# Kernel optimization log

Measured on AMD Instinct MI355X. Metric: run time of the kernel, lower is better.

The kernel has to match this reference:

```python
import jax, jax.numpy as jnp
import numpy as np

EPS_LN = 1e-6
EPS_BN = 1e-5
NUM_HEADS = 8


def _dwconv(img, w, b=None, stride=1):
    # img: (B,C,H,W), w: (C,1,k,k) depthwise
    out = jax.lax.conv_general_dilated(
        img, w, (stride, stride), 'SAME',
        feature_group_count=img.shape[1],
        dimension_numbers=('NCHW', 'OIHW', 'NCHW'))
    if b is not None:
        out = out + b[None, :, None, None]
    return out


def _layernorm(x, g, b):
    m = jnp.mean(x, axis=-1, keepdims=True)
    v = jnp.mean(jnp.square(x - m), axis=-1, keepdims=True)
    return (x - m) * jax.lax.rsqrt(v + EPS_LN) * g + b


def _hardswish(x):
    return x * jnp.clip(x + 3.0, 0.0, 6.0) * (1.0 / 6.0)


def _forward(img, domain_label, pe_dw_w, pe_pw_w, pe_bn_g, pe_bn_b, pe_bn_m, pe_bn_v,
             cpe_w, cpe_b, norm1_g, norm1_b, qkv_w, qkv_b,
             crpe_w3, crpe_b3, crpe_w5, crpe_b5, crpe_w7, crpe_b7,
             dom_w1, dom_b1, dom_w2, dom_b2, proj_w, proj_b,
             norm2_g, norm2_b, fc1_w, fc1_b, fc2_w, fc2_b, d):
    B = img.shape[0]
    # --- DWCPatchEmbed_M: depthwise 3x3 s2 + pointwise 1x1 + domain BN (eval) + hardswish ---
    x = _dwconv(img, pe_dw_w, None, stride=2)                      # (B,Cin,H,W)
    x = jax.lax.conv_general_dilated(x, pe_pw_w, (1, 1), 'SAME',
                                     dimension_numbers=('NCHW', 'OIHW', 'NCHW'))
    g, be, mu, var = pe_bn_g[d], pe_bn_b[d], pe_bn_m[d], pe_bn_v[d]
    scale_bn = g * jax.lax.rsqrt(var + EPS_BN)
    x = (x - mu[None, :, None, None]) * scale_bn[None, :, None, None] + be[None, :, None, None]
    x = _hardswish(x)
    _, C, H, W = x.shape
    N = H * W
    x = x.reshape(B, C, N).transpose(0, 2, 1)                      # (B,N,C) tokens

    # --- ConvPosEnc: depthwise 3x3 on image layout, residual ---
    img2 = x.transpose(0, 2, 1).reshape(B, C, H, W)
    x = x + _dwconv(img2, cpe_w, cpe_b).reshape(B, C, N).transpose(0, 2, 1)

    # --- FactorAtt_ConvRelPosEnc_Sup ---
    cur = _layernorm(x, norm1_g[d], norm1_b[d])
    h = NUM_HEADS
    Ch = C // h
    qkv = cur @ qkv_w + qkv_b                                      # (B,N,3C)
    qkv = qkv.reshape(B, N, 3, h, Ch).transpose(2, 0, 3, 1, 4)     # (3,B,h,N,Ch)
    q, k, v = qkv[0], qkv[1], qkv[2]
    k_sm = jax.nn.softmax(k, axis=2)                               # softmax over tokens
    kv = jnp.einsum('bhnk,bhnv->bhkv', k_sm, v)                    # (B,h,Ch,Ch)
    factor_att = jnp.einsum('bhnk,bhkv->bhnv', q, kv)              # (B,h,N,Ch)

    # conv relative position encoding: windows {3:2heads, 5:3heads, 7:3heads}
    v_img = v.transpose(0, 1, 3, 2).reshape(B, C, H, W)            # (B, h*Ch, H, W)
    s1, s2 = 2 * Ch, 5 * Ch
    cv = jnp.concatenate([
        _dwconv(v_img[:, :s1], crpe_w3, crpe_b3),
        _dwconv(v_img[:, s1:s2], crpe_w5, crpe_b5),
        _dwconv(v_img[:, s2:], crpe_w7, crpe_b7)], axis=1)
    cv = cv.reshape(B, h, Ch, N).transpose(0, 1, 3, 2)             # (B,h,N,Ch)
    crpe = q * cv

    factor_att = (Ch ** -0.5) * factor_att + crpe

    # domain gate: Linear->ReLU->Linear on one-hot, softmax over heads
    da = jax.nn.relu(domain_label @ dom_w1 + dom_b1) @ dom_w2 + dom_b2   # (B,C)
    da = da.reshape(B, h, Ch)[:, :, None, :]                        # (B,h,1,Ch)
    da = jax.nn.softmax(da, axis=1)
    out = da * factor_att                                           # (B,h,N,Ch)
    out = out.transpose(0, 2, 1, 3).reshape(B, N, C)
    out = out @ proj_w + proj_b
    x = x + out

    # --- MLP (ratio 8), domain LayerNorm, residual ---
    cur = _layernorm(x, norm2_g[d], norm2_b[d])
    cur = jax.nn.gelu(cur @ fc1_w + fc1_b, approximate=False) @ fc2_w + fc2_b
    x = x + cur
    return x


def setup_inputs() -> dict:
    key = jax.random.key(0)
    ks = jax.random.split(key, 16)
    B, Cin, Hin, Win = 8, 64, 128, 128
    C, h, D = 128, NUM_HEADS, 4
    Ch = C // h
    hid_dom = C // 2
    hid_mlp = 8 * C
    f = jnp.float32

    def n(k, shape, s=0.02):
        return (s * jax.random.normal(k, shape)).astype(f)

    img = jax.random.normal(ks[0], (B, Cin, Hin, Win), dtype=f)
    domain_label = jax.nn.one_hot(jnp.zeros((B,), jnp.int32), D, dtype=f)
    return dict(
        img=img, domain_label=domain_label,
        pe_dw_w=n(ks[1], (Cin, 1, 3, 3), 0.1),
        pe_pw_w=n(ks[2], (C, Cin, 1, 1), 0.1),
        pe_bn_g=jnp.ones((D, C), f), pe_bn_b=jnp.zeros((D, C), f),
        pe_bn_m=n(ks[3], (D, C), 0.1),
        pe_bn_v=jnp.ones((D, C), f),
        cpe_w=n(ks[4], (C, 1, 3, 3), 0.1), cpe_b=jnp.zeros((C,), f),
        norm1_g=jnp.ones((D, C), f), norm1_b=jnp.zeros((D, C), f),
        qkv_w=n(ks[5], (C, 3 * C)), qkv_b=jnp.zeros((3 * C,), f),
        crpe_w3=n(ks[6], (2 * Ch, 1, 3, 3), 0.1), crpe_b3=jnp.zeros((2 * Ch,), f),
        crpe_w5=n(ks[7], (3 * Ch, 1, 5, 5), 0.1), crpe_b5=jnp.zeros((3 * Ch,), f),
        crpe_w7=n(ks[8], (3 * Ch, 1, 7, 7), 0.1), crpe_b7=jnp.zeros((3 * Ch,), f),
        dom_w1=n(ks[9], (D, hid_dom)), dom_b1=jnp.zeros((hid_dom,), f),
        dom_w2=n(ks[10], (hid_dom, C)), dom_b2=jnp.zeros((C,), f),
        proj_w=n(ks[11], (C, C)), proj_b=jnp.zeros((C,), f),
        norm2_g=jnp.ones((D, C), f), norm2_b=jnp.zeros((D, C), f),
        fc1_w=n(ks[12], (C, hid_mlp)), fc1_b=jnp.zeros((hid_mlp,), f),
        fc2_w=n(ks[13], (hid_mlp, C)), fc2_b=jnp.zeros((C,), f),
        d=0,
    )


def reference(img, domain_label, pe_dw_w, pe_pw_w, pe_bn_g, pe_bn_b, pe_bn_m, pe_bn_v,
              cpe_w, cpe_b, norm1_g, norm1_b, qkv_w, qkv_b,
              crpe_w3, crpe_b3, crpe_w5, crpe_b5, crpe_w7, crpe_b7,
              dom_w1, dom_b1, dom_w2, dom_b2, proj_w, proj_b,
              norm2_g, norm2_b, fc1_w, fc1_b, fc2_w, fc2_b, d):
    return _forward(img, domain_label, pe_dw_w, pe_pw_w, pe_bn_g, pe_bn_b, pe_bn_m, pe_bn_v,
                    cpe_w, cpe_b, norm1_g, norm1_b, qkv_w, qkv_b,
                    crpe_w3, crpe_b3, crpe_w5, crpe_b5, crpe_w7, crpe_b7,
                    dom_w1, dom_b1, dom_w2, dom_b2, proj_w, proj_b,
                    norm2_g, norm2_b, fc1_w, fc1_b, fc2_w, fc2_b, d)
```

## Files before the change

### kernel.cpp

```cpp
#include <hip/hip_runtime.h>
#include <math.h>

#define EPS_LN 1e-6f
#define EPS_BN 1e-5f

typedef __attribute__((ext_vector_type(8))) short bf16x8;
typedef __attribute__((ext_vector_type(4))) float f32x4;

__device__ __forceinline__ float wave_reduce_sum(float v) {
    #pragma unroll
    for (int m = 32; m >= 1; m >>= 1) v += __shfl_xor(v, m, 64);
    return v;
}
__device__ __forceinline__ float wave_reduce_max(float v) {
    #pragma unroll
    for (int m = 32; m >= 1; m >>= 1) v = fmaxf(v, __shfl_xor(v, m, 64));
    return v;
}
__device__ __forceinline__ short f2bf(float f) {
    union { float f; unsigned u; } v; v.f = f;
    unsigned r = v.u + 0x7fff + ((v.u >> 16) & 1);
    return (short)(r >> 16);
}
__device__ __forceinline__ unsigned pack2bf(float a, float b) {
    return (unsigned)(unsigned short)f2bf(a) | ((unsigned)(unsigned short)f2bf(b) << 16);
}

__global__ __launch_bounds__(256) void pe_kernel(
    const float* __restrict__ img, const float* __restrict__ dww,
    const float* __restrict__ pww, const float* __restrict__ bn_g,
    const float* __restrict__ bn_b, const float* __restrict__ bn_m,
    const float* __restrict__ bn_v, const int* __restrict__ dptr,
    float* __restrict__ t1) {
    __shared__ float dw[64 * 68];
    __shared__ float wsm[64 * 132];
    int bx = blockIdx.x;
    int b = bx >> 6, y = bx & 63;
    int tid = threadIdx.x;
    int d = *dptr;

    for (int idx = tid; idx < 8192; idx += 256) {
        int co = idx >> 6, ci = idx & 63;
        wsm[ci * 132 + co] = pww[idx];
    }

    for (int it = 0; it < 4; ++it) {
        int task = tid + it * 256;
        int ci = task >> 4, xx0 = (task & 15) * 4;
        const float* ip = img + (size_t)(b * 64 + ci) * 16384;
        const float* wd = dww + ci * 9;
        float a0 = 0.f, a1 = 0.f, a2 = 0.f, a3 = 0.f;
        #pragma unroll
        for (int r = 0; r < 3; ++r) {
            int iy = 2 * y + r;
            if (iy >= 128) continue;
            const float* rp = ip + iy * 128 + 2 * xx0;
            float u[9];
            *(f32x4*)&u[0] = *(const f32x4*)rp;
            *(f32x4*)&u[4] = *(const f32x4*)(rp + 4);
            u[8] = (xx0 < 60) ? rp[8] : 0.f;
            #pragma unroll
            for (int s = 0; s < 3; ++s) {
                float w = wd[r * 3 + s];
                a0 += u[s] * w;
                a1 += u[2 + s] * w;
                a2 += u[4 + s] * w;
                a3 += u[6 + s] * w;
            }
        }
        f32x4 st = {a0, a1, a2, a3};
        *(f32x4*)&dw[ci * 68 + xx0] = st;
    }
    __syncthreads();

    int xg = tid & 15, cog = tid >> 4;
    int xx0 = xg * 4, co0 = cog * 8;
    f32x4 acc[8];
    f32x4 zr = {0.f, 0.f, 0.f, 0.f};
    #pragma unroll
    for (int i = 0; i < 8; ++i) acc[i] = zr;
    for (int ci = 0; ci < 64; ++ci) {
        f32x4 dv = *(const f32x4*)&dw[ci * 68 + xx0];
        f32x4 w0 = *(const f32x4*)&wsm[ci * 132 + co0];
        f32x4 w1 = *(const f32x4*)&wsm[ci * 132 + co0 + 4];
        acc[0] += dv * w0.x; acc[1] += dv * w0.y;
        acc[2] += dv * w0.z; acc[3] += dv * w0.w;
        acc[4] += dv * w1.x; acc[5] += dv * w1.y;
        acc[6] += dv * w1.z; acc[7] += dv * w1.w;
    }
    #pragma unroll
    for (int i = 0; i < 8; ++i) {
        int co = co0 + i;
        float sc = bn_g[d * 128 + co] * rsqrtf(bn_v[d * 128 + co] + EPS_BN);
        float mu = bn_m[d * 128 + co], be = bn_b[d * 128 + co];
        f32x4 v = (acc[i] - mu) * sc + be;
        f32x4 r;
        r.x = v.x * fminf(fmaxf(v.x + 3.f, 0.f), 6.f) * (1.f / 6.f);
        r.y = v.y * fminf(fmaxf(v.y + 3.f, 0.f), 6.f) * (1.f / 6.f);
        r.z = v.z * fminf(fmaxf(v.z + 3.f, 0.f), 6.f) * (1.f / 6.f);
        r.w = v.w * fminf(fmaxf(v.w + 3.f, 0.f), 6.f) * (1.f / 6.f);
        *(f32x4*)&t1[(size_t)(b * 128 + co) * 4096 + y * 64 + xx0] = r;
    }
}

__global__ __launch_bounds__(256) void cpe_kernel(
    const float* __restrict__ t1, const float* __restrict__ cw,
    const float* __restrict__ cb, float* __restrict__ xout) {
    int bx = blockIdx.x;
    int cq = bx & 3, y = (bx >> 2) & 63, b = bx >> 8;
    int c0 = cq * 32;
    __shared__ float s[3 * 32 * 65];
    int tid = threadIdx.x;
    for (int idx = tid; idx < 3 * 32 * 64; idx += 256) {
        int xx = idx & 63;
        int cl = (idx >> 6) & 31;
        int dy = idx >> 11;
        int yy = y + dy - 1;
        float v = 0.f;
        if (yy >= 0 && yy < 64)
            v = t1[(size_t)(b * 128 + c0 + cl) * 4096 + yy * 64 + xx];
        s[(dy * 32 + cl) * 65 + xx] = v;
    }
    __syncthreads();
    for (int idx = tid; idx < 32 * 64; idx += 256) {
        int cl = idx & 31;
        int xx = idx >> 5;
        int c = c0 + cl;
        float center = s[(32 + cl) * 65 + xx];
        float acc = cb[c];
        #pragma unroll
        for (int dy = 0; dy < 3; ++dy) {
            #pragma unroll
            for (int dx = 0; dx < 3; ++dx) {
                int sx = xx + dx - 1;
                if (sx < 0 || sx >= 64) continue;
                acc += s[(dy * 32 + cl) * 65 + sx] * cw[c * 9 + dy * 3 + dx];
            }
        }
        xout[(size_t)(b * 4096 + y * 64 + xx) * 128 + c] = center + acc;
    }
}

__global__ __launch_bounds__(256) void pack_qkv_kernel(
    const float* __restrict__ w, const float* __restrict__ g,
    const int* __restrict__ dptr, short* __restrict__ wp) {
    int idx = blockIdx.x * 256 + threadIdx.x;
    int d = *dptr;
    int l = idx & 63, kk = (idx >> 6) & 3, n = idx >> 8;
    int k0 = kk * 32 + (l >> 4) * 8;
    int c = n * 16 + (l & 15);
    bf16x8 v;
    #pragma unroll
    for (int j = 0; j < 8; ++j)
        v[j] = f2bf(g[d * 128 + k0 + j] * w[(size_t)(k0 + j) * 384 + c]);
    *(bf16x8*)&wp[(size_t)idx * 8] = v;
}
__global__ __launch_bounds__(256) void pack_pw_kernel(
    const float* __restrict__ w, short* __restrict__ wp) {
    int idx = blockIdx.x * 256 + threadIdx.x;
    int l = idx & 63, kk = (idx >> 6) & 3, n = idx >> 8;
    int k0 = kk * 32 + (l >> 4) * 8;
    int c = n * 16 + (l & 15);
    bf16x8 v;
    #pragma unroll
    for (int j = 0; j < 8; ++j) v[j] = f2bf(w[(size_t)(k0 + j) * 128 + c]);
    *(bf16x8*)&wp[(size_t)idx * 8] = v;
}
__global__ __launch_bounds__(256) void pack_w1_kernel(
    const float* __restrict__ w1, const float* __restrict__ g,
    const int* __restrict__ dptr, short* __restrict__ w1p) {
    int idx = blockIdx.x * 256 + threadIdx.x;
    int d = *dptr;
    int l = idx & 63, kk = (idx >> 6) & 3, n = idx >> 8;
    int k0 = kk * 32 + (l >> 4) * 8;
    int c = n * 16 + (l & 15);
    bf16x8 v;
    #pragma unroll
    for (int j = 0; j < 8; ++j)
        v[j] = f2bf(g[d * 128 + k0 + j] * w1[(size_t)(k0 + j) * 1024 + c]);
    *(bf16x8*)&w1p[(size_t)idx * 8] = v;
}
__global__ __launch_bounds__(256) void pack_w2_kernel(
    const float* __restrict__ w2, short* __restrict__ w2p) {
    int idx = blockIdx.x * 256 + threadIdx.x;
    int l = idx & 63, kk = (idx >> 6) & 31, n = idx >> 11;
    int k0 = kk * 32 + (l >> 4) * 8;
    int c = n * 16 + (l & 15);
    bf16x8 v;
    #pragma unroll
    for (int j = 0; j < 8; ++j) v[j] = f2bf(w2[(size_t)(k0 + j) * 128 + c]);
    *(bf16x8*)&w2p[(size_t)idx * 8] = v;
}

__global__ __launch_bounds__(256) void fold_qkv_bias_kernel(
    const float* __restrict__ w, const float* __restrict__ bqkv,
    const float* __restrict__ beta, const int* __restrict__ dptr,
    float* __restrict__ bp) {
    int j = blockIdx.x * 256 + threadIdx.x;
    if (j >= 384) return;
    int d = *dptr;
    float s = bqkv[j];
    for (int k = 0; k < 128; ++k) s += beta[d * 128 + k] * w[(size_t)k * 384 + j];
    bp[j] = s;
}
__global__ __launch_bounds__(256) void fold_fc1_bias_kernel(
    const float* __restrict__ w, const float* __restrict__ b1,
    const float* __restrict__ beta, const int* __restrict__ dptr,
    float* __restrict__ bp) {
    int j = blockIdx.x * 256 + threadIdx.x;
    if (j >= 1024) return;
    int d = *dptr;
    float s = b1[j];
    for (int k = 0; k < 128; ++k) s += beta[d * 128 + k] * w[(size_t)k * 1024 + j];
    bp[j] = s;
}

__global__ __launch_bounds__(256, 2) void qkv_mfma_kernel(
    const float* __restrict__ x, const short* __restrict__ wp,
    const float* __restrict__ biasp, float* __restrict__ q_img,
    float* __restrict__ k_img, float* __restrict__ v_img) {
    int tb = blockIdx.x * 32;
    int tid = threadIdx.x;
    int lane = tid & 63, wv = tid >> 6;
    int lhi = lane >> 4, llo = lane & 15;
    int b = tb >> 12, n0 = tb & 4095;

    bf16x8 afr[2][4];
    #pragma unroll
    for (int tt = 0; tt < 2; ++tt) {
        f32x4 v0[4], v1[4];
        float sum = 0.f;
        #pragma unroll
        for (int kk = 0; kk < 4; ++kk) {
            const float* p = x + (size_t)(tb + tt * 16 + llo) * 128 + kk * 32 + lhi * 8;
            v0[kk] = *(const f32x4*)p;
            v1[kk] = *(const f32x4*)(p + 4);
            sum += v0[kk].x + v0[kk].y + v0[kk].z + v0[kk].w
                 + v1[kk].x + v1[kk].y + v1[kk].z + v1[kk].w;
        }
        sum += __shfl_xor(sum, 16, 64);
        sum += __shfl_xor(sum, 32, 64);
        float mean = sum * (1.f / 128.f);
        float vs = 0.f;
        #pragma unroll
        for (int kk = 0; kk < 4; ++kk) {
            f32x4 a = v0[kk], c = v1[kk];
            float d0 = a.x - mean, d1 = a.y - mean, d2 = a.z - mean, d3 = a.w - mean;
            float d4 = c.x - mean, d5 = c.y - mean, d6 = c.z - mean, d7 = c.w - mean;
            vs += d0*d0 + d1*d1 + d2*d2 + d3*d3 + d4*d4 + d5*d5 + d6*d6 + d7*d7;
        }
        vs += __shfl_xor(vs, 16, 64);
        vs += __shfl_xor(vs, 32, 64);
        float rs = rsqrtf(vs * (1.f / 128.f) + EPS_LN);
        #pragma unroll
        for (int kk = 0; kk < 4; ++kk) {
            bf16x8 o;
            o[0] = f2bf((v0[kk].x - mean) * rs);
            o[1] = f2bf((v0[kk].y - mean) * rs);
            o[2] = f2bf((v0[kk].z - mean) * rs);
            o[3] = f2bf((v0[kk].w - mean) * rs);
            o[4] = f2bf((v1[kk].x - mean) * rs);
            o[5] = f2bf((v1[kk].y - mean) * rs);
            o[6] = f2bf((v1[kk].z - mean) * rs);
            o[7] = f2bf((v1[kk].w - mean) * rs);
            afr[tt][kk] = o;
        }
    }

    f32x4 acc[6][2];
    f32x4 zr = {0.f, 0.f, 0.f, 0.f};
    #pragma unroll
    for (int i = 0; i < 6; ++i) { acc[i][0] = zr; acc[i][1] = zr; }

    #pragma unroll
    for (int i = 0; i < 6; ++i) {
        int nb = wv * 6 + i;
        #pragma unroll
        for (int kk = 0; kk < 4; ++kk) {
            bf16x8 wf = *(const bf16x8*)&wp[((size_t)(nb * 4 + kk) * 64 + lane) * 8];
            acc[i][0] = __builtin_amdgcn_mfma_f32_16x16x32_bf16(wf, afr[0][kk], acc[i][0], 0, 0, 0);
            acc[i][1] = __builtin_amdgcn_mfma_f32_16x16x32_bf16(wf, afr[1][kk], acc[i][1], 0, 0, 0);
        }
    }

    #pragma unroll
    for (int i = 0; i < 6; ++i) {
        int j0 = (wv * 6 + i) * 16;
        f32x4 bv = *(const f32x4*)(biasp + j0 + lhi * 4);
        float* dst = (j0 < 128) ? q_img : ((j0 < 256) ? k_img : v_img);
        int c0 = (j0 & 127) + lhi * 4;
        #pragma unroll
        for (int tt = 0; tt < 2; ++tt) {
            f32x4 r = acc[i][tt] + bv;
            float* p = dst + (size_t)(b * 128 + c0) * 4096 + n0 + tt * 16 + llo;
            p[0]        = r.x;
            p[4096]     = r.y;
            p[2 * 4096] = r.z;
            p[3 * 4096] = r.w;
        }
    }
}

__global__ __launch_bounds__(256) void softmax_kernel(float* __restrict__ k_img) {
    __shared__ float red[4];
    float* p = k_img + (size_t)blockIdx.x * 4096;
    int tid = threadIdx.x;
    float v[16];
    float mx = -1e30f;
    #pragma unroll
    for (int i = 0; i < 16; ++i) {
        v[i] = p[tid + i * 256];
        mx = fmaxf(mx, v[i]);
    }
    mx = wave_reduce_max(mx);
    int wid = tid >> 6, lane = tid & 63;
    if (lane == 0) red[wid] = mx;
    __syncthreads();
    mx = fmaxf(fmaxf(red[0], red[1]), fmaxf(red[2], red[3]));
    __syncthreads();
    float sum = 0.f;
    #pragma unroll
    for (int i = 0; i < 16; ++i) {
        v[i] = expf(v[i] - mx);
        sum += v[i];
    }
    sum = wave_reduce_sum(sum);
    if (lane == 0) red[wid] = sum;
    __syncthreads();
    float inv = 1.f / (red[0] + red[1] + red[2] + red[3]);
    #pragma unroll
    for (int i = 0; i < 16; ++i)
        p[tid + i * 256] = v[i] * inv;
}

__global__ __launch_bounds__(256) void kv_part_kernel(
    const float* __restrict__ k_img, const float* __restrict__ v_img,
    float* __restrict__ kvp) {
    __shared__ float ks[16 * 132], vs[16 * 132];
    int bc = blockIdx.x;
    int bh = bc >> 3, chunk = bc & 7;
    int b = bh >> 3, h = bh & 7;
    int tid = threadIdx.x;
    int ck = tid >> 4, cv = tid & 15;
    float acc = 0.f;
    const float* kp = k_img + (size_t)(b * 128 + h * 16) * 4096;
    const float* vp = v_img + (size_t)(b * 128 + h * 16) * 4096;
    int nb0 = chunk * 512;
    for (int nb = nb0; nb < nb0 + 512; nb += 128) {
        for (int idx = tid; idx < 2048; idx += 256) {
            int r = idx >> 7, col = idx & 127;
            ks[r * 132 + col] = kp[(size_t)r * 4096 + nb + col];
            vs[r * 132 + col] = vp[(size_t)r * 4096 + nb + col];
        }
        __syncthreads();
        for (int kk = 0; kk < 128; ++kk)
            acc += ks[ck * 132 + kk] * vs[cv * 132 + kk];
        __syncthreads();
    }
    kvp[(size_t)(chunk * 64 + bh) * 256 + ck * 16 + cv] = acc;
}
__global__ __launch_bounds__(256) void kv_reduce_kernel(
    const float* __restrict__ kvp, float* __restrict__ kv) {
    int i = blockIdx.x * 256 + threadIdx.x;
    float s = 0.f;
    #pragma unroll
    for (int c = 0; c < 8; ++c) s += kvp[(size_t)c * 16384 + i];
    kv[i] = s;
}

__global__ __launch_bounds__(256) void fa_kernel(
    const float* __restrict__ q_img, const float* __restrict__ kv,
    float* __restrict__ fa_img) {
    __shared__ float kvs[256];
    int bid = blockIdx.x;
    int bh = bid >> 4, chunk = bid & 15;
    int b = bh >> 3, h = bh & 7;
    int tid = threadIdx.x;
    kvs[tid] = kv[bh * 256 + tid];
    __syncthreads();
    int n = chunk * 256 + tid;
    const float* qp = q_img + (size_t)(b * 128 + h * 16) * 4096 + n;
    float qv[16];
    #pragma unroll
    for (int ck = 0; ck < 16; ++ck) qv[ck] = qp[(size_t)ck * 4096];
    float* fp = fa_img + (size_t)(b * 128 + h * 16) * 4096 + n;
    #pragma unroll
    for (int cv = 0; cv < 16; ++cv) {
        float s = 0.f;
        #pragma unroll
        for (int ck = 0; ck < 16; ++ck) s += qv[ck] * kvs[ck * 16 + cv];
        fp[(size_t)cv * 4096] = s;
    }
}

__global__ __launch_bounds__(256) void gate_kernel(
    const float* __restrict__ dl, const float* __restrict__ w1,
    const float* __restrict__ b1, const float* __restrict__ w2,
    const float* __restrict__ b2, float* __restrict__ da) {
    __shared__ float hid[512];
    __shared__ float raw[1024];
    int tid = threadIdx.x;
    for (int idx = tid; idx < 512; idx += 256) {
        int b = idx >> 6, jj = idx & 63;
        float a = b1[jj];
        #pragma unroll
        for (int dd = 0; dd < 4; ++dd)
            a += dl[b * 4 + dd] * w1[dd * 64 + jj];
        hid[idx] = fmaxf(a, 0.f);
    }
    __syncthreads();
    for (int idx = tid; idx < 1024; idx += 256) {
        int b = idx >> 7, c = idx & 127;
        float a = b2[c];
        for (int jj = 0; jj < 64; ++jj)
            a += hid[b * 64 + jj] * w2[jj * 128 + c];
        raw[idx] = a;
    }
    __syncthreads();
    if (tid < 128) {
        int b = tid >> 4, ch = tid & 15;
        float mx = -1e30f;
        #pragma unroll
        for (int hh = 0; hh < 8; ++hh)
            mx = fmaxf(mx, raw[b * 128 + hh * 16 + ch]);
        float e[8];
        float s = 0.f;
        #pragma unroll
        for (int hh = 0; hh < 8; ++hh) {
            e[hh] = expf(raw[b * 128 + hh * 16 + ch] - mx);
            s += e[hh];
        }
        float inv = 1.f / s;
        #pragma unroll
        for (int hh = 0; hh < 8; ++hh)
            da[b * 128 + hh * 16 + ch] = e[hh] * inv;
    }
}

template<int KC>
__device__ __forceinline__ void conv4(const float* __restrict__ s,
                                      const float* __restrict__ wsm,
                                      int y, int xx0, float* a4) {
    const int OFF = KC / 2;
    #pragma unroll
    for (int dy = 0; dy < KC; ++dy) {
        int sy = y + dy - OFF;
        if (sy < 0 || sy >= 64) continue;
        const float* r = s + sy * 72;
        float u[12];
        *(f32x4*)&u[0] = *(const f32x4*)&r[xx0];
        *(f32x4*)&u[4] = *(const f32x4*)&r[xx0 + 4];
        *(f32x4*)&u[8] = *(const f32x4*)&r[xx0 + 8];
        #pragma unroll
        for (int dx = 0; dx < KC; ++dx) {
            float w = wsm[dy * KC + dx];
            const int base = dx - OFF + 4;
            a4[0] += u[base + 0] * w;
            a4[1] += u[base + 1] * w;
            a4[2] += u[base + 2] * w;
            a4[3] += u[base + 3] * w;
        }
    }
}

__global__ __launch_bounds__(256) void att_kernel(
    const float* __restrict__ q_img, const float* __restrict__ v_img,
    const float* __restrict__ fa_img, const float* __restrict__ da,
    const float* __restrict__ w3, const float* __restrict__ b3,
    const float* __restrict__ w5, const float* __restrict__ b5,
    const float* __restrict__ w7, const float* __restrict__ b7,
    float* __restrict__ att) {
    __shared__ float s[64 * 72];
    __shared__ float wsm[49];
    int o = ((blockIdx.x & 7) << 7) | (blockIdx.x >> 3);
    int b = o >> 7, c = o & 127;
    int tid = threadIdx.x;
    const float* vp = v_img + (size_t)(b * 128 + c) * 4096;
    for (int idx = tid; idx < 4096; idx += 256) {
        int row = idx >> 6, xx = idx & 63;
        s[row * 72 + xx + 4] = vp[idx];
    }
    for (int idx = tid; idx < 512; idx += 256) {
        int row = idx >> 3, j = idx & 7;
        s[row * 72 + (j < 4 ? j : 64 + j)] = 0.f;
    }
    int kc; const float* wp; float bias;
    if (c < 32)      { kc = 3; wp = w3 + c * 9;         bias = b3[c]; }
    else if (c < 80) { kc = 5; wp = w5 + (c - 32) * 25; bias = b5[c - 32]; }
    else             { kc = 7; wp = w7 + (c - 80) * 49; bias = b7[c - 80]; }
    if (tid < kc * kc) wsm[tid] = wp[tid];
    float dac = da[b * 128 + c];
    size_t rowbase = (size_t)(b * 128 + c) * 4096;
    __syncthreads();
    for (int it = 0; it < 4; ++it) {
        int task = tid + it * 256;
        int y = task >> 4, xx0 = (task & 15) * 4;
        float a4[4] = {bias, bias, bias, bias};
        if (kc == 3)      conv4<3>(s, wsm, y, xx0, a4);
        else if (kc == 5) conv4<5>(s, wsm, y, xx0, a4);
        else              conv4<7>(s, wsm, y, xx0, a4);
        size_t base = rowbase + y * 64 + xx0;
        f32x4 fav = *(const f32x4*)&fa_img[base];
        f32x4 qv  = *(const f32x4*)&q_img[base];
        f32x4 cv4 = {a4[0], a4[1], a4[2], a4[3]};
        f32x4 r = (fav * 0.25f + qv * cv4) * dac;
        *(f32x4*)&att[base] = r;
    }
}

__global__ __launch_bounds__(256, 2) void proj_mfma_kernel(
    const float* __restrict__ att, const short* __restrict__ wp,
    const float* __restrict__ bias, const float* __restrict__ xres,
    float* __restrict__ out) {
    __shared__ float As[128 * 33];
    int tb = blockIdx.x * 32;
    int tid = threadIdx.x;
    int lane = tid & 63, wv = tid >> 6;
    int lhi = lane >> 4, llo = lane & 15;
    int b = tb >> 12, n0 = tb & 4095;

    for (int idx = tid; idx < 4096; idx += 256) {
        int c = idx >> 5, t = idx & 31;
        As[c * 33 + t] = att[(size_t)(b * 128 + c) * 4096 + n0 + t];
    }
    __syncthreads();

    bf16x8 afr[2][4];
    #pragma unroll
    for (int tt = 0; tt < 2; ++tt) {
        #pragma unroll
        for (int kk = 0; kk < 4; ++kk) {
            int c0 = kk * 32 + lhi * 8;
            int t = tt * 16 + llo;
            bf16x8 v;
            #pragma unroll
            for (int j = 0; j < 8; ++j) v[j] = f2bf(As[(c0 + j) * 33 + t]);
            afr[tt][kk] = v;
        }
    }

    f32x4 acc[2][2];
    f32x4 zr = {0.f, 0.f, 0.f, 0.f};
    #pragma unroll
    for (int i = 0; i < 2; ++i) { acc[i][0] = zr; acc[i][1] = zr; }

    #pragma unroll
    for (int i = 0; i < 2; ++i) {
        int nb = wv * 2 + i;
        #pragma unroll
        for (int kk = 0; kk < 4; ++kk) {
            bf16x8 wf = *(const bf16x8*)&wp[((size_t)(nb * 4 + kk) * 64 + lane) * 8];
            acc[i][0] = __builtin_amdgcn_mfma_f32_16x16x32_bf16(wf, afr[0][kk], acc[i][0], 0, 0, 0);
            acc[i][1] = __builtin_amdgcn_mfma_f32_16x16x32_bf16(wf, afr[1][kk], acc[i][1], 0, 0, 0);
        }
    }

    #pragma unroll
    for (int i = 0; i < 2; ++i) {
        int j0 = (wv * 2 + i) * 16;
        f32x4 bv = *(const f32x4*)(bias + j0 + lhi * 4);
        #pragma unroll
        for (int tt = 0; tt < 2; ++tt) {
            size_t o = (size_t)(tb + tt * 16 + llo) * 128 + j0 + lhi * 4;
            f32x4 xr = *(const f32x4*)(xres + o);
            *(f32x4*)(out + o) = xr + acc[i][tt] + bv;
        }
    }
}

__global__ __launch_bounds__(256, 2) void mlp_mfma_kernel(
    const short* __restrict__ w1p, const float* __restrict__ b1p,
    const short* __restrict__ w2p, const float* __restrict__ b2,
    float* io) {
    __shared__ short hs[32768];
    int tb = blockIdx.x * 32;
    int tid = threadIdx.x;
    int lane = tid & 63, wv = tid >> 6;
    int lhi = lane >> 4, llo = lane & 15;

    bf16x8 afr[2][4];
    #pragma unroll
    for (int tt = 0; tt < 2; ++tt) {
        f32x4 v0[4], v1[4];
        float sum = 0.f;
        #pragma unroll
        for (int kk = 0; kk < 4; ++kk) {
            const float* p = io + (size_t)(tb + tt * 16 + llo) * 128 + kk * 32 + lhi * 8;
            v0[kk] = *(const f32x4*)p;
            v1[kk] = *(const f32x4*)(p + 4);
            sum += v0[kk].x + v0[kk].y + v0[kk].z + v0[kk].w
                 + v1[kk].x + v1[kk].y + v1[kk].z + v1[kk].w;
        }
        sum += __shfl_xor(sum, 16, 64);
        sum += __shfl_xor(sum, 32, 64);
        float mean = sum * (1.f / 128.f);
        float vs = 0.f;
        #pragma unroll
        for (int kk = 0; kk < 4; ++kk) {
            f32x4 a = v0[kk], c = v1[kk];
            float d0 = a.x - mean, d1 = a.y - mean, d2 = a.z - mean, d3 = a.w - mean;
            float d4 = c.x - mean, d5 = c.y - mean, d6 = c.z - mean, d7 = c.w - mean;
            vs += d0*d0 + d1*d1 + d2*d2 + d3*d3 + d4*d4 + d5*d5 + d6*d6 + d7*d7;
        }
        vs += __shfl_xor(vs, 16, 64);
        vs += __shfl_xor(vs, 32, 64);
        float rs = rsqrtf(vs * (1.f / 128.f) + EPS_LN);
        #pragma unroll
        for (int kk = 0; kk < 4; ++kk) {
            bf16x8 o;
            o[0] = f2bf((v0[kk].x - mean) * rs);
            o[1] = f2bf((v0[kk].y - mean) * rs);
            o[2] = f2bf((v0[kk].z - mean) * rs);
            o[3] = f2bf((v0[kk].w - mean) * rs);
            o[4] = f2bf((v1[kk].x - mean) * rs);
            o[5] = f2bf((v1[kk].y - mean) * rs);
            o[6] = f2bf((v1[kk].z - mean) * rs);
            o[7] = f2bf((v1[kk].w - mean) * rs);
            afr[tt][kk] = o;
        }
    }

    f32x4 acc[2][16];
    f32x4 zr = {0.f, 0.f, 0.f, 0.f};
    #pragma unroll
    for (int tt = 0; tt < 2; ++tt)
        #pragma unroll
        for (int nl = 0; nl < 16; ++nl) acc[tt][nl] = zr;

    const short* wbase = w1p + (size_t)(wv * 16) * 4 * 64 * 8;
    #pragma unroll
    for (int nl = 0; nl < 16; ++nl) {
        #pragma unroll
        for (int kk = 0; kk < 4; ++kk) {
            bf16x8 bf = *(const bf16x8*)(wbase + ((size_t)(nl * 4 + kk) * 64 + lane) * 8);
            acc[0][nl] = __builtin_amdgcn_mfma_f32_16x16x32_bf16(bf, afr[0][kk], acc[0][nl], 0, 0, 0);
            acc[1][nl] = __builtin_amdgcn_mfma_f32_16x16x32_bf16(bf, afr[1][kk], acc[1][nl], 0, 0, 0);
        }
    }

    #pragma unroll
    for (int nl = 0; nl < 16; ++nl) {
        int hn = wv * 16 + nl;
        int hc0 = hn * 16 + lhi * 4;
        f32x4 bv = *(const f32x4*)(b1p + hc0);
        int kk2 = hn >> 1;
        int lp = llo + 16 * ((hn & 1) * 2 + (lhi >> 1));
        #pragma unroll
        for (int tt = 0; tt < 2; ++tt) {
            f32x4 a = acc[tt][nl] + bv;
            float g0 = 0.5f * a.x * (1.f + erff(a.x * 0.70710678118654752f));
            float g1 = 0.5f * a.y * (1.f + erff(a.y * 0.70710678118654752f));
            float g2 = 0.5f * a.z * (1.f + erff(a.z * 0.70710678118654752f));
            float g3 = 0.5f * a.w * (1.f + erff(a.w * 0.70710678118654752f));
            uint2 wv2;
            wv2.x = pack2bf(g0, g1);
            wv2.y = pack2bf(g2, g3);
            *(uint2*)((char*)hs + ((size_t)(tt * 32 + kk2) * 64 + lp) * 16 + (lhi & 1) * 8) = wv2;
        }
    }
    __syncthreads();

    f32x4 acc2[2][2];
    #pragma unroll
    for (int cn = 0; cn < 2; ++cn)
        #pragma unroll
        for (int tt = 0; tt < 2; ++tt) acc2[cn][tt] = zr;

    const short* w2base = w2p + (size_t)(wv * 2) * 32 * 64 * 8;
    #pragma unroll 4
    for (int kk2 = 0; kk2 < 32; ++kk2) {
        bf16x8 h0 = *(const bf16x8*)&hs[((size_t)(0 * 32 + kk2) * 64 + lane) * 8];
        bf16x8 h1 = *(const bf16x8*)&hs[((size_t)(1 * 32 + kk2) * 64 + lane) * 8];
        bf16x8 w0 = *(const bf16x8*)(w2base + ((size_t)(0 * 32 + kk2) * 64 + lane) * 8);
        bf16x8 w1f = *(const bf16x8*)(w2base + ((size_t)(1 * 32 + kk2) * 64 + lane) * 8);
        acc2[0][0] = __builtin_amdgcn_mfma_f32_16x16x32_bf16(w0, h0, acc2[0][0], 0, 0, 0);
        acc2[0][1] = __builtin_amdgcn_mfma_f32_16x16x32_bf16(w0, h1, acc2[0][1], 0, 0, 0);
        acc2[1][0] = __builtin_amdgcn_mfma_f32_16x16x32_bf16(w1f, h0, acc2[1][0], 0, 0, 0);
        acc2[1][1] = __builtin_amdgcn_mfma_f32_16x16x32_bf16(w1f, h1, acc2[1][1], 0, 0, 0);
    }

    #pragma unroll
    for (int cn = 0; cn < 2; ++cn) {
        int c0 = (wv * 2 + cn) * 16 + lhi * 4;
        f32x4 bv = *(const f32x4*)(b2 + c0);
        #pragma unroll
        for (int tt = 0; tt < 2; ++tt) {
            float* op = io + (size_t)(tb + tt * 16 + llo) * 128 + c0;
            f32x4 r = *(f32x4*)op;
            r = r + acc2[cn][tt] + bv;
            *(f32x4*)op = r;
        }
    }
}

extern "C" void kernel_launch(void* const* d_in, const int* in_sizes, int n_in,
                              void* d_out, int out_size, void* d_ws, size_t ws_size,
                              hipStream_t stream) {
    const float* img   = (const float*)d_in[0];
    const float* dl    = (const float*)d_in[1];
    const float* pe_dw = (const float*)d_in[2];
    const float* pe_pw = (const float*)d_in[3];
    const float* bn_g  = (const float*)d_in[4];
    const float* bn_b  = (const float*)d_in[5];
    const float* bn_m  = (const float*)d_in[6];
    const float* bn_v  = (const float*)d_in[7];
    const float* cpe_w = (const float*)d_in[8];
    const float* cpe_b = (const float*)d_in[9];
    const float* n1_g  = (const float*)d_in[10];
    const float* n1_b  = (const float*)d_in[11];
    const float* qkv_w = (const float*)d_in[12];
    const float* qkv_b = (const float*)d_in[13];
    const float* w3    = (const float*)d_in[14];
    const float* b3    = (const float*)d_in[15];
    const float* w5    = (const float*)d_in[16];
    const float* b5    = (const float*)d_in[17];
    const float* w7    = (const float*)d_in[18];
    const float* b7    = (const float*)d_in[19];
    const float* dw1   = (const float*)d_in[20];
    const float* db1   = (const float*)d_in[21];
    const float* dw2   = (const float*)d_in[22];
    const float* db2   = (const float*)d_in[23];
    const float* pw    = (const float*)d_in[24];
    const float* pb    = (const float*)d_in[25];
    const float* n2_g  = (const float*)d_in[26];
    const float* n2_b  = (const float*)d_in[27];
    const float* f1w   = (const float*)d_in[28];
    const float* f1b   = (const float*)d_in[29];
    const float* f2w   = (const float*)d_in[30];
    const float* f2b   = (const float*)d_in[31];
    const int*   dptr  = (const int*)d_in[32];
    float* out = (float*)d_out;

    char* ws = (char*)d_ws;
    const size_t SZ = (size_t)8 * 128 * 4096 * 4;
    float* t1    = (float*)(ws);
    float* x     = (float*)(ws + SZ);
    float* q_img = (float*)(ws + 2 * SZ);
    float* k_img = (float*)(ws + 3 * SZ);
    float* v_img = (float*)(ws + 4 * SZ);
    float* kv    = (float*)(ws + 5 * SZ);
    float* da    = (float*)(ws + 5 * SZ + 0x10000);
    short* qkvp  = (short*)(ws + 5 * SZ + 0x20000);
    short* pwp   = (short*)(ws + 5 * SZ + 0x40000);
    float* qbp   = (float*)(ws + 5 * SZ + 0x48000);
    float* f1bp  = (float*)(ws + 5 * SZ + 0x4A000);
    float* kvp   = (float*)(ws + 5 * SZ + 0x50000);
    float* fa_img = t1;
    short* w1p   = (short*)(ws + 2 * SZ);
    short* w2p   = (short*)(ws + 2 * SZ + 262144);

    pack_qkv_kernel<<<24, 256, 0, stream>>>(qkv_w, n1_g, dptr, qkvp);
    fold_qkv_bias_kernel<<<2, 256, 0, stream>>>(qkv_w, qkv_b, n1_b, dptr, qbp);
    pack_pw_kernel<<<8, 256, 0, stream>>>(pw, pwp);
    gate_kernel<<<1, 256, 0, stream>>>(dl, dw1, db1, dw2, db2, da);
    pe_kernel<<<512, 256, 0, stream>>>(img, pe_dw, pe_pw, bn_g, bn_b, bn_m, bn_v, dptr, t1);
    cpe_kernel<<<2048, 256, 0, stream>>>(t1, cpe_w, cpe_b, x);
    qkv_mfma_kernel<<<1024, 256, 0, stream>>>(x, qkvp, qbp, q_img, k_img, v_img);
    softmax_kernel<<<1024, 256, 0, stream>>>(k_img);
    kv_part_kernel<<<512, 256, 0, stream>>>(k_img, v_img, kvp);
    kv_reduce_kernel<<<64, 256, 0, stream>>>(kvp, kv);
    fa_kernel<<<1024, 256, 0, stream>>>(q_img, kv, fa_img);
    att_kernel<<<1024, 256, 0, stream>>>(q_img, v_img, fa_img, da, w3, b3, w5, b5, w7, b7, k_img);
    proj_mfma_kernel<<<1024, 256, 0, stream>>>(k_img, pwp, pb, x, out);
    pack_w1_kernel<<<64, 256, 0, stream>>>(f1w, n2_g, dptr, w1p);
    fold_fc1_bias_kernel<<<4, 256, 0, stream>>>(f1w, f1b, n2_b, dptr, f1bp);
    pack_w2_kernel<<<64, 256, 0, stream>>>(f2w, w2p);
    mlp_mfma_kernel<<<1024, 256, 0, stream>>>(w1p, f1bp, w2p, f2b, out);
}
```

Baseline: 379.6 us.

## Split QKV and MLP MFMA kernels across 8 waves, one token tile each

The QKV and MLP fused GEMM kernels now launch 512 threads per block instead of 256. Each wave handles one of the two 16-token sub-tiles rather than both, which halves the per-wave accumulator and A-fragment registers and aims for more waves resident per CU. In exchange, each weight fragment is loaded by two waves instead of being reused across both token tiles in registers, so weight traffic roughly doubles and LayerNorm work is split, not shared.

Result: faster. 367.6 us (-3.2%).

```diff
diff --git a/kernel.cpp b/kernel.cpp
--- a/kernel.cpp
+++ b/kernel.cpp
@@ -215,19 +215,19 @@
     bp[j] = s;
 }
 
-__global__ __launch_bounds__(256, 2) void qkv_mfma_kernel(
+__global__ __launch_bounds__(512, 4) void qkv_mfma_kernel(
     const float* __restrict__ x, const short* __restrict__ wp,
     const float* __restrict__ biasp, float* __restrict__ q_img,
     float* __restrict__ k_img, float* __restrict__ v_img) {
     int tb = blockIdx.x * 32;
     int tid = threadIdx.x;
     int lane = tid & 63, wv = tid >> 6;
+    int tt = wv & 1, g = wv >> 1;
     int lhi = lane >> 4, llo = lane & 15;
     int b = tb >> 12, n0 = tb & 4095;
 
-    bf16x8 afr[2][4];
-    #pragma unroll
-    for (int tt = 0; tt < 2; ++tt) {
+    bf16x8 afr[4];
+    {
         f32x4 v0[4], v1[4];
         float sum = 0.f;
         #pragma unroll
@@ -263,41 +263,37 @@
             o[5] = f2bf((v1[kk].y - mean) * rs);
             o[6] = f2bf((v1[kk].z - mean) * rs);
             o[7] = f2bf((v1[kk].w - mean) * rs);
-            afr[tt][kk] = o;
-        }
-    }
-
-    f32x4 acc[6][2];
+            afr[kk] = o;
+        }
+    }
+
+    f32x4 acc[6];
     f32x4 zr = {0.f, 0.f, 0.f, 0.f};
     #pragma unroll
-    for (int i = 0; i < 6; ++i) { acc[i][0] = zr; acc[i][1] = zr; }
+    for (int i = 0; i < 6; ++i) acc[i] = zr;
 
     #pragma unroll
     for (int i = 0; i < 6; ++i) {
-        int nb = wv * 6 + i;
+        int nb = g * 6 + i;
         #pragma unroll
         for (int kk = 0; kk < 4; ++kk) {
             bf16x8 wf = *(const bf16x8*)&wp[((size_t)(nb * 4 + kk) * 64 + lane) * 8];
-            acc[i][0] = __builtin_amdgcn_mfma_f32_16x16x32_bf16(wf, afr[0][kk], acc[i][0], 0, 0, 0);
-            acc[i][1] = __builtin_amdgcn_mfma_f32_16x16x32_bf16(wf, afr[1][kk], acc[i][1], 0, 0, 0);
+            acc[i] = __builtin_amdgcn_mfma_f32_16x16x32_bf16(wf, afr[kk], acc[i], 0, 0, 0);
         }
     }
 
     #pragma unroll
     for (int i = 0; i < 6; ++i) {
-        int j0 = (wv * 6 + i) * 16;
+        int j0 = (g * 6 + i) * 16;
         f32x4 bv = *(const f32x4*)(biasp + j0 + lhi * 4);
         float* dst = (j0 < 128) ? q_img : ((j0 < 256) ? k_img : v_img);
         int c0 = (j0 & 127) + lhi * 4;
-        #pragma unroll
-        for (int tt = 0; tt < 2; ++tt) {
-            f32x4 r = acc[i][tt] + bv;
-            float* p = dst + (size_t)(b * 128 + c0) * 4096 + n0 + tt * 16 + llo;
-            p[0]        = r.x;
-            p[4096]     = r.y;
-            p[2 * 4096] = r.z;
-            p[3 * 4096] = r.w;
-        }
+        f32x4 r = acc[i] + bv;
+        float* p = dst + (size_t)(b * 128 + c0) * 4096 + n0 + tt * 16 + llo;
+        p[0]        = r.x;
+        p[4096]     = r.y;
+        p[2 * 4096] = r.z;
+        p[3 * 4096] = r.w;
     }
 }
 
@@ -568,7 +564,7 @@
     }
 }
 
-__global__ __launch_bounds__(256, 2) void mlp_mfma_kernel(
+__global__ __launch_bounds__(512, 4) void mlp_mfma_kernel(
     const short* __restrict__ w1p, const float* __restrict__ b1p,
     const short* __restrict__ w2p, const float* __restrict__ b2,
     float* io) {
@@ -576,11 +572,11 @@
     int tb = blockIdx.x * 32;
     int tid = threadIdx.x;
     int lane = tid & 63, wv = tid >> 6;
+    int tt = wv & 1, g = wv >> 1;
     int lhi = lane >> 4, llo = lane & 15;
 
-    bf16x8 afr[2][4];
-    #pragma unroll
-    for (int tt = 0; tt < 2; ++tt) {
+    bf16x8 afr[4];
+    {
         f32x4 v0[4], v1[4];
         float sum = 0.f;
         #pragma unroll
@@ -616,80 +612,65 @@
             o[5] = f2bf((v1[kk].y - mean) * rs);
             o[6] = f2bf((v1[kk].z - mean) * rs);
             o[7] = f2bf((v1[kk].w - mean) * rs);
-            afr[tt][kk] = o;
-        }
-    }
-
-    f32x4 acc[2][16];
+            afr[kk] = o;
+        }
+    }
+
+    f32x4 acc[16];
     f32x4 zr = {0.f, 0.f, 0.f, 0.f};
     #pragma unroll
-    for (int tt = 0; tt < 2; ++tt)
-        #pragma unroll
-        for (int nl = 0; nl < 16; ++nl) acc[tt][nl] = zr;
-
-    const short* wbase = w1p + (size_t)(wv * 16) * 4 * 64 * 8;
+    for (int nl = 0; nl < 16; ++nl) acc[nl] = zr;
+
+    const short* wbase = w1p + (size_t)(g * 16) * 4 * 64 * 8;
     #pragma unroll
     for (int nl = 0; nl < 16; ++nl) {
         #pragma unroll
         for (int kk = 0; kk < 4; ++kk) {
             bf16x8 bf = *(const bf16x8*)(wbase + ((size_t)(nl * 4 + kk) * 64 + lane) * 8);
-            acc[0][nl] = __builtin_amdgcn_mfma_f32_16x16x32_bf16(bf, afr[0][kk], acc[0][nl], 0, 0, 0);
-            acc[1][nl] = __builtin_amdgcn_mfma_f32_16x16x32_bf16(bf, afr[1][kk], acc[1][nl], 0, 0, 0);
+            acc[nl] = __builtin_amdgcn_mfma_f32_16x16x32_bf16(bf, afr[kk], acc[nl], 0, 0, 0);
         }
     }
 
     #pragma unroll
     for (int nl = 0; nl < 16; ++nl) {
-        int hn = wv * 16 + nl;
+        int hn = g * 16 + nl;
         int hc0 = hn * 16 + lhi * 4;
         f32x4 bv = *(const f32x4*)(b1p + hc0);
         int kk2 = hn >> 1;
         int lp = llo + 16 * ((hn & 1) * 2 + (lhi >> 1));
-        #pragma unroll
-        for (int tt = 0; tt < 2; ++tt) {
-            f32x4 a = acc[tt][nl] + bv;
-            float g0 = 0.5f * a.x * (1.f + erff(a.x * 0.70710678118654752f));
-            float g1 = 0.5f * a.y * (1.f + erff(a.y * 0.70710678118654752f));
-            float g2 = 0.5f * a.z * (1.f + erff(a.z * 0.70710678118654752f));
-            float g3 = 0.5f * a.w * (1.f + erff(a.w * 0.70710678118654752f));
-            uint2 wv2;
-            wv2.x = pack2bf(g0, g1);
-            wv2.y = pack2bf(g2, g3);
-            *(uint2*)((char*)hs + ((size_t)(tt * 32 + kk2) * 64 + lp) * 16 + (lhi & 1) * 8) = wv2;
-        }
-    }
-    __syncthreads();
-
-    f32x4 acc2[2][2];
-    #pragma unroll
-    for (int cn = 0; cn < 2; ++cn)
-        #pragma unroll
-        for (int tt = 0; tt < 2; ++tt) acc2[cn][tt] = zr;
-
-    const short* w2base = w2p + (size_t)(wv * 2) * 32 * 64 * 8;
+        f32x4 a = acc[nl] + bv;
+        float g0 = 0.5f * a.x * (1.f + erff(a.x * 0.70710678118654752f));
+        float g1 = 0.5f * a.y * (1.f + erff(a.y * 0.70710678118654752f));
+        float g2 = 0.5f * a.z * (1.f + erff(a.z * 0.70710678118654752f));
+        float g3 = 0.5f * a.w * (1.f + erff(a.w * 0.70710678118654752f));
+        uint2 wv2;
+        wv2.x = pack2bf(g0, g1);
+        wv2.y = pack2bf(g2, g3);
+        *(uint2*)((char*)hs + ((size_t)(tt * 32 + kk2) * 64 + lp) * 16 + (lhi & 1) * 8) = wv2;
+    }
+    __syncthreads();
+
+    f32x4 acc2[2];
+    acc2[0] = zr; acc2[1] = zr;
+
+    const short* w2base = w2p + (size_t)wv * 32 * 64 * 8;
     #pragma unroll 4
     for (int kk2 = 0; kk2 < 32; ++kk2) {
         bf16x8 h0 = *(const bf16x8*)&hs[((size_t)(0 * 32 + kk2) * 64 + lane) * 8];
         bf16x8 h1 = *(const bf16x8*)&hs[((size_t)(1 * 32 + kk2) * 64 + lane) * 8];
-        bf16x8 w0 = *(const bf16x8*)(w2base + ((size_t)(0 * 32 + kk2) * 64 + lane) * 8);
-        bf16x8 w1f = *(const bf16x8*)(w2base + ((size_t)(1 * 32 + kk2) * 64 + lane) * 8);
-        acc2[0][0] = __builtin_amdgcn_mfma_f32_16x16x32_bf16(w0, h0, acc2[0][0], 0, 0, 0);
-        acc2[0][1] = __builtin_amdgcn_mfma_f32_16x16x32_bf16(w0, h1, acc2[0][1], 0, 0, 0);
-        acc2[1][0] = __builtin_amdgcn_mfma_f32_16x16x32_bf16(w1f, h0, acc2[1][0], 0, 0, 0);
-        acc2[1][1] = __builtin_amdgcn_mfma_f32_16x16x32_bf16(w1f, h1, acc2[1][1], 0, 0, 0);
-    }
-
-    #pragma unroll
-    for (int cn = 0; cn < 2; ++cn) {
-        int c0 = (wv * 2 + cn) * 16 + lhi * 4;
-        f32x4 bv = *(const f32x4*)(b2 + c0);
-        #pragma unroll
-        for (int tt = 0; tt < 2; ++tt) {
-            float* op = io + (size_t)(tb + tt * 16 + llo) * 128 + c0;
-            f32x4 r = *(f32x4*)op;
-            r = r + acc2[cn][tt] + bv;
-            *(f32x4*)op = r;
-        }
+        bf16x8 w0 = *(const bf16x8*)(w2base + ((size_t)kk2 * 64 + lane) * 8);
+        acc2[0] = __builtin_amdgcn_mfma_f32_16x16x32_bf16(w0, h0, acc2[0], 0, 0, 0);
+        acc2[1] = __builtin_amdgcn_mfma_f32_16x16x32_bf16(w0, h1, acc2[1], 0, 0, 0);
+    }
+
+    int c0 = wv * 16 + lhi * 4;
+    f32x4 bv = *(const f32x4*)(b2 + c0);
+    #pragma unroll
+    for (int tt2 = 0; tt2 < 2; ++tt2) {
+        float* op = io + (size_t)(tb + tt2 * 16 + llo) * 128 + c0;
+        f32x4 r = *(f32x4*)op;
+        r = r + acc2[tt2] + bv;
+        *(f32x4*)op = r;
     }
 }
 
@@ -755,7 +736,7 @@
     gate_kernel<<<1, 256, 0, stream>>>(dl, dw1, db1, dw2, db2, da);
     pe_kernel<<<512, 256, 0, stream>>>(img, pe_dw, pe_pw, bn_g, bn_b, bn_m, bn_v, dptr, t1);
     cpe_kernel<<<2048, 256, 0, stream>>>(t1, cpe_w, cpe_b, x);
-    qkv_mfma_kernel<<<1024, 256, 0, stream>>>(x, qkvp, qbp, q_img, k_img, v_img);
+    qkv_mfma_kernel<<<1024, 512, 0, stream>>>(x, qkvp, qbp, q_img, k_img, v_img);
     softmax_kernel<<<1024, 256, 0, stream>>>(k_img);
     kv_part_kernel<<<512, 256, 0, stream>>>(k_img, v_img, kvp);
     kv_reduce_kernel<<<64, 256, 0, stream>>>(kvp, kv);
@@ -765,5 +746,5 @@
     pack_w1_kernel<<<64, 256, 0, stream>>>(f1w, n2_g, dptr, w1p);
     fold_fc1_bias_kernel<<<4, 256, 0, stream>>>(f1w, f1b, n2_b, dptr, f1bp);
     pack_w2_kernel<<<64, 256, 0, stream>>>(f2w, w2p);
-    mlp_mfma_kernel<<<1024, 256, 0, stream>>>(w1p, f1bp, w2p, f2b, out);
-}
+    mlp_mfma_kernel<<<1024, 512, 0, stream>>>(w1p, f1bp, w2p, f2b, out);
+}
```
